# Performance work log

Hardware: AMD Instinct MI355X
Metric: run time of the kernel (lower is better)

Reference implementation:

```python
import jax, jax.numpy as jnp
import numpy as np

NPOINT = 2048
K = 16
EPS = 1e-5


def farthest_point_sample(xyz, npoint):
    # xyz: (B, N, 3) -> (B, npoint) int32 indices. Deterministic start at index 0.
    B, N, _ = xyz.shape
    batch = jnp.arange(B)

    def step(carry, _):
        dists, far = carry                      # (B,N), (B,)
        centroid = xyz[batch, far]              # (B,3)
        d = jnp.sum((xyz - centroid[:, None, :]) ** 2, axis=-1)  # (B,N)
        dists = jnp.minimum(dists, d)
        nxt = jnp.argmax(dists, axis=-1).astype(jnp.int32)
        return (dists, nxt), far

    init = (jnp.full((B, N), 1e10, xyz.dtype), jnp.zeros((B,), jnp.int32))
    _, idx = jax.lax.scan(step, init, None, length=npoint)
    return jnp.transpose(idx)                   # (B, npoint)


def knn_query(k, xyz, query_xyz):
    # squared-distance KNN via matmul form (same ordering as torch.cdist+topk smallest)
    x2 = jnp.sum(xyz * xyz, axis=-1)            # (B,N)
    q2 = jnp.sum(query_xyz * query_xyz, axis=-1)  # (B,S)
    sqd = q2[:, :, None] + x2[:, None, :] - 2.0 * jnp.einsum('bsd,bnd->bsn', query_xyz, xyz)
    _, idx = jax.lax.top_k(-sqd, k)             # smallest k distances
    return idx                                  # (B,S,k)


def layer_norm(x, g, b):
    mu = jnp.mean(x, axis=-1, keepdims=True)
    var = jnp.mean((x - mu) ** 2, axis=-1, keepdims=True)
    return (x - mu) * jax.lax.rsqrt(var + EPS) * g + b


def setup_inputs() -> dict:
    key = jax.random.key(0)
    ks = jax.random.split(key, 6)
    B, N, IN_DIM, OUT_DIM = 4, 8192, 64, 128
    C_IN = 3 + IN_DIM
    s1 = 1.0 / np.sqrt(C_IN)
    s2 = 1.0 / np.sqrt(OUT_DIM)
    return {
        'xyz': jax.random.normal(ks[0], (B, N, 3), jnp.float32),
        'feat': jax.random.normal(ks[1], (B, N, IN_DIM), jnp.float32),
        'W1': jax.random.uniform(ks[2], (C_IN, OUT_DIM), jnp.float32, -s1, s1),
        'b1': jax.random.uniform(ks[3], (OUT_DIM,), jnp.float32, -s1, s1),
        'W2': jax.random.uniform(ks[4], (OUT_DIM, OUT_DIM), jnp.float32, -s2, s2),
        'b2': jax.random.uniform(ks[5], (OUT_DIM,), jnp.float32, -s2, s2),
        'ln_g': jnp.ones((OUT_DIM,), jnp.float32),
        'ln_b': jnp.zeros((OUT_DIM,), jnp.float32),
    }


def reference(xyz, feat, W1, b1, W2, b2, ln_g, ln_b):
    B = xyz.shape[0]
    bidx = jnp.arange(B)[:, None, None]

    fps_idx = farthest_point_sample(xyz, NPOINT)                 # (B,S)
    new_xyz = jnp.take_along_axis(xyz, fps_idx[:, :, None], axis=1)  # (B,S,3)
    knn_idx = knn_query(K, xyz, new_xyz)                         # (B,S,K)

    grp_xyz = xyz[bidx, knn_idx] - new_xyz[:, :, None, :]        # (B,S,K,3)
    grp_feat = feat[bidx, knn_idx]                               # (B,S,K,in_dim)
    grouped = jnp.concatenate([grp_xyz, grp_feat], axis=-1)      # (B,S,K,3+in_dim)

    h = jax.nn.relu(grouped @ W1 + b1)
    h = h @ W2 + b2                                              # (B,S,K,out_dim)
    new_feat = jnp.max(h, axis=2)                                # (B,S,out_dim)
    return new_xyz, layer_norm(new_feat, ln_g, ln_b)
```

## Files before the change

### kernel.cpp

```cpp
#include <hip/hip_runtime.h>
#include <stdint.h>

#define BB 4
#define NN 8192
#define SS 2048
#define KK 16
#define IND 64
#define CIN 67
#define OD 128

typedef unsigned int   u32;
typedef unsigned long long u64;
typedef float f2 __attribute__((ext_vector_type(2)));

#define TAG 0x5EED0000u
#define CW  252
#define GRID (BB + CW)
#define NWAVES (CW*8)
#define SLICE 3632
#define DYN_LDS (8*SLICE*4)

__global__ __launch_bounds__(256) void k_prep(const float* __restrict__ xyz,
                                              float4* __restrict__ pts,
                                              u32* __restrict__ progress){
  if (blockIdx.x==0 && threadIdx.x<BB) progress[threadIdx.x] = 0u;
  int i = blockIdx.x * 256 + threadIdx.x;
  if (i >= BB*NN) return;
  float x = xyz[3*i+0];
  float y = xyz[3*i+1];
  float z = xyz[3*i+2];
  float x2 = __fadd_rn(__fadd_rn(__fmul_rn(x,x), __fmul_rn(y,y)), __fmul_rn(z,z));
  pts[i] = make_float4(x,y,z,x2);
}

template<int CTRL>
__device__ __forceinline__ float dpp_mv(float x){
  int xi = __builtin_bit_cast(int, x);
  int r  = __builtin_amdgcn_update_dpp(xi, xi, CTRL, 0xf, 0xf, false);
  return __builtin_bit_cast(float, r);
}

#define FPT 512
#define PPT (NN/FPT)
#define NW  (FPT/64)
__global__ __launch_bounds__(512) void k_fused(const float4* __restrict__ pts,
                                               float* __restrict__ out_xyz,
                                               const float* __restrict__ feat,
                                               const float* __restrict__ W1, const float* __restrict__ b1,
                                               const float* __restrict__ W2, const float* __restrict__ b2,
                                               const float* __restrict__ g_ln, const float* __restrict__ b_ln,
                                               float* __restrict__ out_feat,
                                               u32* __restrict__ progress){
  extern __shared__ float smem[];
  __shared__ u64 pkey[2][NW];
  int tid = threadIdx.x;
  int wid = tid >> 6, lane = tid & 63;

  if (blockIdx.x < BB){
    #pragma clang fp contract(off)
    float* sx = smem;
    float* sy = smem +   NN;
    float* sz = smem + 2*NN;
    int b = blockIdx.x;
    const float4* P = pts + (size_t)b*NN;
    f2 X[PPT/2], Y[PPT/2], Z[PPT/2], D[PPT/2];
    #pragma unroll
    for (int jp=0;jp<PPT/2;jp++){
      int n0 = tid*PPT + 2*jp;
      float4 p0 = P[n0];
      float4 p1 = P[n0+1];
      X[jp] = (f2){p0.x, p1.x};
      Y[jp] = (f2){p0.y, p1.y};
      Z[jp] = (f2){p0.z, p1.z};
      D[jp] = (f2){1e10f, 1e10f};
      sx[n0]=p0.x; sx[n0+1]=p1.x;
      sy[n0]=p0.y; sy[n0+1]=p1.y;
      sz[n0]=p0.z; sz[n0+1]=p1.z;
    }
    float4 p0v = P[0];
    float cx=p0v.x, cy=p0v.y, cz=p0v.z;
    size_t ob = (size_t)b*SS*3;
    if (tid==1){
      out_xyz[ob+0]=cx; out_xyz[ob+1]=cy; out_xyz[ob+2]=cz;
      __hip_atomic_store(&progress[b], TAG|0u, __ATOMIC_RELEASE, __HIP_MEMORY_SCOPE_AGENT);
    }
    __syncthreads();

    for (int it=1; it<SS; ++it){
      f2 mm0 = (f2){-1.0f, -1.0f}, mm1 = (f2){-1.0f, -1.0f};
      #pragma unroll
      for (int jp=0;jp<PPT/2;jp+=2){
        f2 dx0 = X[jp] - cx,   dy0 = Y[jp] - cy,   dz0 = Z[jp] - cz;
        f2 dx1 = X[jp+1] - cx, dy1 = Y[jp+1] - cy, dz1 = Z[jp+1] - cz;
        f2 d0  = ((dx0*dx0) + (dy0*dy0)) + (dz0*dz0);
        f2 d1  = ((dx1*dx1) + (dy1*dy1)) + (dz1*dz1);
        f2 nd0 = __builtin_elementwise_min(D[jp],   d0);
        f2 nd1 = __builtin_elementwise_min(D[jp+1], d1);
        D[jp]   = nd0;
        D[jp+1] = nd1;
        mm0 = __builtin_elementwise_max(mm0, nd0);
        mm1 = __builtin_elementwise_max(mm1, nd1);
      }
      f2 mm = __builtin_elementwise_max(mm0, mm1);
      float md = fmaxf(mm.x, mm.y);
      float m = md;
      m = fmaxf(m, dpp_mv<0x111>(m));
      m = fmaxf(m, dpp_mv<0x112>(m));
      m = fmaxf(m, dpp_mv<0x114>(m));
      m = fmaxf(m, dpp_mv<0x118>(m));
      m = fmaxf(m, dpp_mv<0x142>(m));
      m = fmaxf(m, dpp_mv<0x143>(m));
      float wmax = __builtin_bit_cast(float,
          __builtin_amdgcn_readlane(__builtin_bit_cast(int, m), 63));
      u64 ball = __ballot(md == wmax);
      int wl = __ffsll((unsigned long long)ball) - 1;
      if (lane == wl){
        int bj = 0;
        #pragma unroll
        for (int t=PPT-1;t>=0;--t){
          float v = (t&1)? D[t>>1].y : D[t>>1].x;
          if (v == wmax) bj = t;
        }
        int widx = tid*PPT + bj;
        pkey[it&1][wid] = ((u64)__float_as_uint(wmax) << 32) | (u32)~(u32)widx;
      }
      __syncthreads();
      u64 bk = pkey[it&1][0];
      #pragma unroll
      for (int w=1;w<NW;w++){
        u64 k2 = pkey[it&1][w];
        if (k2 > bk) bk = k2;
      }
      int gw = (int)~(u32)bk;
      cx = sx[gw]; cy = sy[gw]; cz = sz[gw];
      if (tid==1){
        size_t o = ob + (size_t)it*3;
        out_xyz[o]=cx; out_xyz[o+1]=cy; out_xyz[o+2]=cz;
        if ((it & 15) == 15 || it == SS-1)
          __hip_atomic_store(&progress[b], TAG|(u32)it,
                             __ATOMIC_RELEASE, __HIP_MEMORY_SCOPE_AGENT);
      }
    }
    return;
  }

  int gid = (blockIdx.x - BB)*8 + wid;
  float* gw = smem + wid*SLICE;
  float* hw = gw + CIN*16 + 0;  hw = gw + 1072;
  int k = lane & 15, part = lane >> 4;
  const u32* ctru = (const u32*)out_xyz;

  for (int p = gid; p < BB*SS; p += NWAVES){
    int s = p >> 2, b = p & 3;
    int q = b*SS + s;
    for(;;){
      u32 v = __hip_atomic_load(&progress[b], __ATOMIC_RELAXED, __HIP_MEMORY_SCOPE_AGENT);
      if ((v & 0xFFFF0000u) == TAG && (v & 0xFFFFu) >= (u32)s) break;
      __builtin_amdgcn_s_sleep(64);
    }
    float qx = __builtin_bit_cast(float, __hip_atomic_load(&ctru[3*q+0], __ATOMIC_RELAXED, __HIP_MEMORY_SCOPE_AGENT));
    float qy = __builtin_bit_cast(float, __hip_atomic_load(&ctru[3*q+1], __ATOMIC_RELAXED, __HIP_MEMORY_SCOPE_AGENT));
    float qz = __builtin_bit_cast(float, __hip_atomic_load(&ctru[3*q+2], __ATOMIC_RELAXED, __HIP_MEMORY_SCOPE_AGENT));
    const float4* P = pts + (size_t)b*NN;
    float q2 = __fadd_rn(__fadd_rn(__fmul_rn(qx,qx),__fmul_rn(qy,qy)),__fmul_rn(qz,qz));
    u64 key[KK];
    #pragma unroll
    for (int t=0;t<KK;t++) key[t] = ~0ull;
    for (int i=0;i<NN/64;i++){
      int n = i*64 + lane;
      float4 pp = P[n];
      float dot = __fadd_rn(__fadd_rn(__fmul_rn(qx,pp.x),__fmul_rn(qy,pp.y)),__fmul_rn(qz,pp.z));
      float sd  = __fsub_rn(__fadd_rn(q2,pp.w), __fmul_rn(2.0f,dot));
      u32 bu = __float_as_uint(sd);
      bu ^= (u32)((int)bu >> 31) | 0x80000000u;
      u64 kk = ((u64)bu<<32) | (u32)n;
      if (kk < key[KK-1]){
        key[KK-1] = kk;
        #pragma unroll
        for (int t=KK-1;t>0;--t){
          u64 a=key[t-1], c=key[t];
          bool sw = c < a;
          key[t-1] = sw? c : a;
          key[t]   = sw? a : c;
        }
      }
    }
    int n_sel = 0;
    #pragma unroll 1
    for (int r=0;r<KK;r++){
      u64 m = key[0];
      #pragma unroll
      for (int mm=1;mm<64;mm<<=1){
        u64 om = __shfl_xor((unsigned long long)m, mm, 64);
        if (om < m) m = om;
      }
      if (k == r) n_sel = (int)(u32)m;
      if (key[0]==m){
        #pragma unroll
        for (int t=0;t<KK-1;t++) key[t]=key[t+1];
        key[KK-1]=~0ull;
      }
    }
    {
      const float* fp = feat + ((size_t)b*NN + (size_t)n_sel)*IND + part*16;
      float4 f0 = *(const float4*)(fp+0);
      float4 f1 = *(const float4*)(fp+4);
      float4 f2v = *(const float4*)(fp+8);
      float4 f3 = *(const float4*)(fp+12);
      float v[16] = {f0.x,f0.y,f0.z,f0.w, f1.x,f1.y,f1.z,f1.w,
                     f2v.x,f2v.y,f2v.z,f2v.w, f3.x,f3.y,f3.z,f3.w};
      #pragma unroll
      for (int c=0;c<16;c++) gw[(3+part*16+c)*16 + k] = v[c];
      if (part==0){
        float4 pp = P[n_sel];
        gw[0*16+k] = __fsub_rn(pp.x, qx);
        gw[1*16+k] = __fsub_rn(pp.y, qy);
        gw[2*16+k] = __fsub_rn(pp.z, qz);
      }
    }
    __builtin_amdgcn_wave_barrier();
    int o = lane;
    float a0[16], a1[16];
    #pragma unroll
    for (int t=0;t<16;t++){ a0[t]=0.0f; a1[t]=0.0f; }
    #pragma unroll 4
    for (int j=0;j<CIN;j++){
      float w0 = W1[j*OD + o];
      float w1 = W1[j*OD + o + 64];
      #pragma unroll
      for (int t=0;t<16;t++){
        float gv = gw[j*16+t];
        a0[t]=fmaf(gv,w0,a0[t]); a1[t]=fmaf(gv,w1,a1[t]);
      }
    }
    float bb0 = b1[o], bb1 = b1[o+64];
    #pragma unroll
    for (int t=0;t<16;t++){
      hw[o*20+t]      = fmaxf(a0[t]+bb0, 0.0f);
      hw[(o+64)*20+t] = fmaxf(a1[t]+bb1, 0.0f);
    }
    __builtin_amdgcn_wave_barrier();
    float c0[16], c1[16];
    #pragma unroll
    for (int t=0;t<16;t++){ c0[t]=0.0f; c1[t]=0.0f; }
    #pragma unroll 4
    for (int j=0;j<OD;j++){
      float w0 = W2[j*OD + o];
      float w1 = W2[j*OD + o + 64];
      #pragma unroll
      for (int t=0;t<16;t++){
        float hv = hw[j*20+t];
        c0[t]=fmaf(hv,w0,c0[t]); c1[t]=fmaf(hv,w1,c1[t]);
      }
    }
    float m0=c0[0], m1=c1[0];
    #pragma unroll
    for (int t=1;t<16;t++){ m0=fmaxf(m0,c0[t]); m1=fmaxf(m1,c1[t]); }
    m0 += b2[o]; m1 += b2[o+64];
    float ssum = m0+m1;
    #pragma unroll
    for (int mm=1;mm<64;mm<<=1) ssum += __shfl_xor(ssum,mm,64);
    float mean = ssum * (1.0f/128.0f);
    float d0=m0-mean, d1=m1-mean;
    float sq = d0*d0 + d1*d1;
    #pragma unroll
    for (int mm=1;mm<64;mm<<=1) sq += __shfl_xor(sq,mm,64);
    float var = sq * (1.0f/128.0f);
    float x = var + 1e-5f;
    float r = rsqrtf(x);
    r = r * (1.5f - 0.5f*x*r*r);
    size_t obf = (size_t)q*OD;
    out_feat[obf+o]    = fmaf(d0*r, g_ln[o],    b_ln[o]);
    out_feat[obf+o+64] = fmaf(d1*r, g_ln[o+64], b_ln[o+64]);
  }
}

extern "C" void kernel_launch(void* const* d_in, const int* in_sizes, int n_in,
                              void* d_out, int out_size, void* d_ws, size_t ws_size,
                              hipStream_t stream){
  const float* xyz  = (const float*)d_in[0];
  const float* feat = (const float*)d_in[1];
  const float* W1   = (const float*)d_in[2];
  const float* b1   = (const float*)d_in[3];
  const float* W2   = (const float*)d_in[4];
  const float* b2   = (const float*)d_in[5];
  const float* lg   = (const float*)d_in[6];
  const float* lb   = (const float*)d_in[7];
  float* out = (float*)d_out;
  char* ws = (char*)d_ws;
  float4* pts = (float4*)ws;
  u32*   progress = (u32*)(ws + 524288);
  float* out_xyz  = out;
  float* out_feat = out + (size_t)BB*SS*3;

  hipFuncSetAttribute((const void*)k_fused,
                      hipFuncAttributeMaxDynamicSharedMemorySize, DYN_LDS);

  hipLaunchKernelGGL(k_prep,  dim3((BB*NN+255)/256), dim3(256), 0,       stream, xyz, pts, progress);
  hipLaunchKernelGGL(k_fused, dim3(GRID),            dim3(512), DYN_LDS, stream,
                     pts, out_xyz, feat, W1, b1, W2, b2, lg, lb, out_feat, progress);
}
```

Before: 2.149 ms.

## Drop prep kernel, read raw xyz directly, and batch FPS output writes via LDS ring

```diff
diff --git a/kernel.cpp b/kernel.cpp
--- a/kernel.cpp
+++ b/kernel.cpp
@@ -20,19 +20,6 @@
 #define SLICE 3632
 #define DYN_LDS (8*SLICE*4)
 
-__global__ __launch_bounds__(256) void k_prep(const float* __restrict__ xyz,
-                                              float4* __restrict__ pts,
-                                              u32* __restrict__ progress){
-  if (blockIdx.x==0 && threadIdx.x<BB) progress[threadIdx.x] = 0u;
-  int i = blockIdx.x * 256 + threadIdx.x;
-  if (i >= BB*NN) return;
-  float x = xyz[3*i+0];
-  float y = xyz[3*i+1];
-  float z = xyz[3*i+2];
-  float x2 = __fadd_rn(__fadd_rn(__fmul_rn(x,x), __fmul_rn(y,y)), __fmul_rn(z,z));
-  pts[i] = make_float4(x,y,z,x2);
-}
-
 template<int CTRL>
 __device__ __forceinline__ float dpp_mv(float x){
   int xi = __builtin_bit_cast(int, x);
@@ -43,7 +30,7 @@
 #define FPT 512
 #define PPT (NN/FPT)
 #define NW  (FPT/64)
-__global__ __launch_bounds__(512) void k_fused(const float4* __restrict__ pts,
+__global__ __launch_bounds__(512) void k_fused(const float* __restrict__ xyz,
                                                float* __restrict__ out_xyz,
                                                const float* __restrict__ feat,
                                                const float* __restrict__ W1, const float* __restrict__ b1,
@@ -53,6 +40,7 @@
                                                u32* __restrict__ progress){
   extern __shared__ float smem[];
   __shared__ u64 pkey[2][NW];
+  __shared__ float ring[16*3];
   int tid = threadIdx.x;
   int wid = tid >> 6, lane = tid & 63;
 
@@ -62,26 +50,32 @@
     float* sy = smem +   NN;
     float* sz = smem + 2*NN;
     int b = blockIdx.x;
-    const float4* P = pts + (size_t)b*NN;
+    const float4* Xv = (const float4*)(xyz + (size_t)b*NN*3);
+    float f[48];
+    #pragma unroll
+    for (int v=0;v<12;v++){
+      float4 t4 = Xv[tid*12 + v];
+      f[4*v+0]=t4.x; f[4*v+1]=t4.y; f[4*v+2]=t4.z; f[4*v+3]=t4.w;
+    }
     f2 X[PPT/2], Y[PPT/2], Z[PPT/2], D[PPT/2];
     #pragma unroll
     for (int jp=0;jp<PPT/2;jp++){
-      int n0 = tid*PPT + 2*jp;
-      float4 p0 = P[n0];
-      float4 p1 = P[n0+1];
-      X[jp] = (f2){p0.x, p1.x};
-      Y[jp] = (f2){p0.y, p1.y};
-      Z[jp] = (f2){p0.z, p1.z};
+      int j0 = 2*jp, j1 = 2*jp+1;
+      X[jp] = (f2){f[3*j0+0], f[3*j1+0]};
+      Y[jp] = (f2){f[3*j0+1], f[3*j1+1]};
+      Z[jp] = (f2){f[3*j0+2], f[3*j1+2]};
       D[jp] = (f2){1e10f, 1e10f};
-      sx[n0]=p0.x; sx[n0+1]=p1.x;
-      sy[n0]=p0.y; sy[n0+1]=p1.y;
-      sz[n0]=p0.z; sz[n0+1]=p1.z;
-    }
-    float4 p0v = P[0];
-    float cx=p0v.x, cy=p0v.y, cz=p0v.z;
+      int n0 = tid*PPT + j0;
+      sx[n0]=f[3*j0+0]; sx[n0+1]=f[3*j1+0];
+      sy[n0]=f[3*j0+1]; sy[n0+1]=f[3*j1+1];
+      sz[n0]=f[3*j0+2]; sz[n0+1]=f[3*j1+2];
+    }
+    const float* X0 = xyz + (size_t)b*NN*3;
+    float cx=X0[0], cy=X0[1], cz=X0[2];
     size_t ob = (size_t)b*SS*3;
     if (tid==1){
       out_xyz[ob+0]=cx; out_xyz[ob+1]=cy; out_xyz[ob+2]=cz;
+      ring[0]=cx; ring[1]=cy; ring[2]=cz;
       __hip_atomic_store(&progress[b], TAG|0u, __ATOMIC_RELEASE, __HIP_MEMORY_SCOPE_AGENT);
     }
     __syncthreads();
@@ -134,11 +128,18 @@
       int gw = (int)~(u32)bk;
       cx = sx[gw]; cy = sy[gw]; cz = sz[gw];
       if (tid==1){
-        size_t o = ob + (size_t)it*3;
-        out_xyz[o]=cx; out_xyz[o+1]=cy; out_xyz[o+2]=cz;
-        if ((it & 15) == 15 || it == SS-1)
+        int rs = (it&15)*3;
+        ring[rs]=cx; ring[rs+1]=cy; ring[rs+2]=cz;
+      }
+      if ((it & 15) == 15){
+        if (wid==0 && lane<48){
+          size_t base = ob + (size_t)(it-15)*3;
+          out_xyz[base + lane] = ring[lane];
+        }
+        if (tid==1){
           __hip_atomic_store(&progress[b], TAG|(u32)it,
                              __ATOMIC_RELEASE, __HIP_MEMORY_SCOPE_AGENT);
+        }
       }
     }
     return;
@@ -146,7 +147,7 @@
 
   int gid = (blockIdx.x - BB)*8 + wid;
   float* gw = smem + wid*SLICE;
-  float* hw = gw + CIN*16 + 0;  hw = gw + 1072;
+  float* hw = gw + 1072;
   int k = lane & 15, part = lane >> 4;
   const u32* ctru = (const u32*)out_xyz;
 
@@ -161,16 +162,17 @@
     float qx = __builtin_bit_cast(float, __hip_atomic_load(&ctru[3*q+0], __ATOMIC_RELAXED, __HIP_MEMORY_SCOPE_AGENT));
     float qy = __builtin_bit_cast(float, __hip_atomic_load(&ctru[3*q+1], __ATOMIC_RELAXED, __HIP_MEMORY_SCOPE_AGENT));
     float qz = __builtin_bit_cast(float, __hip_atomic_load(&ctru[3*q+2], __ATOMIC_RELAXED, __HIP_MEMORY_SCOPE_AGENT));
-    const float4* P = pts + (size_t)b*NN;
+    const float* Pb = xyz + (size_t)b*NN*3;
     float q2 = __fadd_rn(__fadd_rn(__fmul_rn(qx,qx),__fmul_rn(qy,qy)),__fmul_rn(qz,qz));
     u64 key[KK];
     #pragma unroll
     for (int t=0;t<KK;t++) key[t] = ~0ull;
     for (int i=0;i<NN/64;i++){
       int n = i*64 + lane;
-      float4 pp = P[n];
-      float dot = __fadd_rn(__fadd_rn(__fmul_rn(qx,pp.x),__fmul_rn(qy,pp.y)),__fmul_rn(qz,pp.z));
-      float sd  = __fsub_rn(__fadd_rn(q2,pp.w), __fmul_rn(2.0f,dot));
+      float px = Pb[3*n], py = Pb[3*n+1], pz = Pb[3*n+2];
+      float x2  = __fadd_rn(__fadd_rn(__fmul_rn(px,px),__fmul_rn(py,py)),__fmul_rn(pz,pz));
+      float dot = __fadd_rn(__fadd_rn(__fmul_rn(qx,px),__fmul_rn(qy,py)),__fmul_rn(qz,pz));
+      float sd  = __fsub_rn(__fadd_rn(q2,x2), __fmul_rn(2.0f,dot));
       u32 bu = __float_as_uint(sd);
       bu ^= (u32)((int)bu >> 31) | 0x80000000u;
       u64 kk = ((u64)bu<<32) | (u32)n;
@@ -212,10 +214,10 @@
       #pragma unroll
       for (int c=0;c<16;c++) gw[(3+part*16+c)*16 + k] = v[c];
       if (part==0){
-        float4 pp = P[n_sel];
-        gw[0*16+k] = __fsub_rn(pp.x, qx);
-        gw[1*16+k] = __fsub_rn(pp.y, qy);
-        gw[2*16+k] = __fsub_rn(pp.z, qz);
+        float ppx = Pb[3*n_sel], ppy = Pb[3*n_sel+1], ppz = Pb[3*n_sel+2];
+        gw[0*16+k] = __fsub_rn(ppx, qx);
+        gw[1*16+k] = __fsub_rn(ppy, qy);
+        gw[2*16+k] = __fsub_rn(ppz, qz);
       }
     }
     __builtin_amdgcn_wave_barrier();
@@ -287,16 +289,14 @@
   const float* lg   = (const float*)d_in[6];
   const float* lb   = (const float*)d_in[7];
   float* out = (float*)d_out;
-  char* ws = (char*)d_ws;
-  float4* pts = (float4*)ws;
-  u32*   progress = (u32*)(ws + 524288);
+  u32* progress = (u32*)d_ws;
   float* out_xyz  = out;
   float* out_feat = out + (size_t)BB*SS*3;
 
   hipFuncSetAttribute((const void*)k_fused,
                       hipFuncAttributeMaxDynamicSharedMemorySize, DYN_LDS);
 
-  hipLaunchKernelGGL(k_prep,  dim3((BB*NN+255)/256), dim3(256), 0,       stream, xyz, pts, progress);
-  hipLaunchKernelGGL(k_fused, dim3(GRID),            dim3(512), DYN_LDS, stream,
-                     pts, out_xyz, feat, W1, b1, W2, b2, lg, lb, out_feat, progress);
+  hipMemsetAsync(progress, 0, BB*sizeof(u32), stream);
+  hipLaunchKernelGGL(k_fused, dim3(GRID), dim3(512), DYN_LDS, stream,
+                     xyz, out_xyz, feat, W1, b1, W2, b2, lg, lb, out_feat, progress);
 }
```

After: 2.138 ms. No clear change (-0.5%).
